# Performance work log

Measured on AMD Instinct MI355X. Metric: run time of the kernel, lower is better.

## Reference

```python
import jax, jax.numpy as jnp
import numpy as np

D = 2048
N_HEAD = 16
D_HEAD = D // N_HEAD
EXP = 4
EPS = 1e-6


def setup_inputs() -> dict:
    key = jax.random.key(0)
    ks = jax.random.split(key, 8)
    b, s = 2, 2048
    scale = 0.02
    return {
        "x": jax.random.normal(ks[0], (b, s, D), dtype=jnp.float32),
        "w_qkv": jax.random.normal(ks[1], (D, 3 * D), dtype=jnp.float32) * scale,
        "w_o": jax.random.normal(ks[2], (D, D), dtype=jnp.float32) * scale,
        "w_up": jax.random.normal(ks[3], (D, EXP * D), dtype=jnp.float32) * scale,
        "w_gate": jax.random.normal(ks[4], (D, EXP * D), dtype=jnp.float32) * scale,
        "w_down": jax.random.normal(ks[5], (EXP * D, D), dtype=jnp.float32) * scale,
        "scale1": jnp.ones((D,), dtype=jnp.float32),
        "scale2": jnp.ones((D,), dtype=jnp.float32),
    }


def _rmsnorm(x, scale):
    rms = jnp.sqrt(jnp.mean(x * x, axis=-1, keepdims=True) + EPS)
    return x / rms * scale


def _attention(x, w_qkv, w_o):
    b, s, d = x.shape
    qkv = x @ w_qkv  # [b, s, 3d]
    q, k, v = jnp.split(qkv, 3, axis=-1)
    # [b, h, s, dh]
    q = q.reshape(b, s, N_HEAD, D_HEAD).transpose(0, 2, 1, 3)
    k = k.reshape(b, s, N_HEAD, D_HEAD).transpose(0, 2, 1, 3)
    v = v.reshape(b, s, N_HEAD, D_HEAD).transpose(0, 2, 1, 3)
    scores = jnp.einsum("bhqd,bhkd->bhqk", q, k) / np.sqrt(D_HEAD).astype(np.float32)
    causal = jnp.tril(jnp.ones((s, s), dtype=bool))
    scores = jnp.where(causal, scores, -jnp.inf)
    attn = jax.nn.softmax(scores, axis=-1)
    out = jnp.einsum("bhqk,bhkd->bhqd", attn, v)
    out = out.transpose(0, 2, 1, 3).reshape(b, s, d)
    return out @ w_o


def _mlp(x, w_up, w_gate, w_down):
    return (x @ w_up * jax.nn.silu(x @ w_gate)) @ w_down


def reference(x, w_qkv, w_o, w_up, w_gate, w_down, scale1, scale2):
    x = x + _attention(_rmsnorm(x, scale1), w_qkv, w_o)
    x = x + _mlp(_rmsnorm(x, scale2), w_up, w_gate, w_down)
    return x
```

## Files before the change

kernel.cpp:

```cpp
#include <hip/hip_runtime.h>

typedef unsigned short u16;
typedef __bf16 bfrag8 __attribute__((ext_vector_type(8)));
typedef float f32x4 __attribute__((ext_vector_type(4)));

#define MFMA16(a, b, c) __builtin_amdgcn_mfma_f32_16x16x32_bf16((a), (b), (c), 0, 0, 0)

static __device__ __forceinline__ u16 bf_bits(float f) {
  unsigned int u = __builtin_bit_cast(unsigned int, f);
  unsigned int r = (u + 0x7fffu + ((u >> 16) & 1u)) >> 16;
  return (u16)r;
}
static __device__ __forceinline__ float f_from_bits(u16 u) {
  unsigned int w = ((unsigned int)u) << 16;
  return __builtin_bit_cast(float, w);
}
static __device__ __forceinline__ void gload16(const void* g, void* l) {
  __builtin_amdgcn_global_load_lds(
      (const __attribute__((address_space(1))) void*)g,
      (__attribute__((address_space(3))) void*)l, 16, 0, 0);
}

__global__ __launch_bounds__(256) void k_transpose_bf16(const float* __restrict__ src,
                                                        u16* __restrict__ dst,
                                                        int K, int N) {
  __shared__ float tile[32][33];
  const int n0 = blockIdx.x * 32;
  const int k0 = blockIdx.y * 32;
  const int t = threadIdx.x;
  const int lr = t >> 5;
  const int lc = t & 31;
#pragma unroll
  for (int i = 0; i < 4; ++i)
    tile[lr + i * 8][lc] = src[(size_t)(k0 + lr + i * 8) * N + n0 + lc];
  __syncthreads();
#pragma unroll
  for (int i = 0; i < 4; ++i)
    dst[(size_t)(n0 + lr + i * 8) * K + k0 + lc] = bf_bits(tile[lc][lr + i * 8]);
}

__global__ __launch_bounds__(256) void k_transpose_v(const u16* __restrict__ qkv,
                                                     u16* __restrict__ vtg) {
  __shared__ u16 tile[32][33];
  const int bh = blockIdx.z, b = bh >> 4, hh = bh & 15;
  const int s0 = blockIdx.x * 32, d0 = blockIdx.y * 32;
  const int t = threadIdx.x;
  const int lr = t >> 5, lc = t & 31;
#pragma unroll
  for (int i = 0; i < 4; ++i)
    tile[lr + i * 8][lc] =
        qkv[(size_t)(b * 2048 + s0 + lr + i * 8) * 6144 + 4096 + hh * 128 + d0 + lc];
  __syncthreads();
#pragma unroll
  for (int i = 0; i < 4; ++i)
    vtg[(size_t)bh * 128 * 2048 + (size_t)(d0 + lr + i * 8) * 2048 + s0 + lc] =
        tile[lc][lr + i * 8];
}

__global__ __launch_bounds__(256) void k_rmsnorm(const float* __restrict__ x,
                                                 const float* __restrict__ sc,
                                                 u16* __restrict__ o) {
  const int row = blockIdx.x;
  const int t = threadIdx.x;
  const float4* x4 = (const float4*)(x + (size_t)row * 2048);
  float4 a = x4[t];
  float4 b = x4[t + 256];
  float ss = a.x * a.x + a.y * a.y + a.z * a.z + a.w * a.w +
             b.x * b.x + b.y * b.y + b.z * b.z + b.w * b.w;
#pragma unroll
  for (int off = 32; off > 0; off >>= 1) ss += __shfl_down(ss, off);
  __shared__ float red[4];
  if ((t & 63) == 0) red[t >> 6] = ss;
  __syncthreads();
  const float inv = rsqrtf((red[0] + red[1] + red[2] + red[3]) * (1.0f / 2048.0f) + 1e-6f);
  const float4* s4 = (const float4*)sc;
  float4 sa = s4[t], sb = s4[t + 256];
  ushort4 pa, pb;
  pa.x = bf_bits(a.x * inv * sa.x); pa.y = bf_bits(a.y * inv * sa.y);
  pa.z = bf_bits(a.z * inv * sa.z); pa.w = bf_bits(a.w * inv * sa.w);
  pb.x = bf_bits(b.x * inv * sb.x); pb.y = bf_bits(b.y * inv * sb.y);
  pb.z = bf_bits(b.z * inv * sb.z); pb.w = bf_bits(b.w * inv * sb.w);
  *(ushort4*)(o + (size_t)row * 2048 + t * 4) = pa;
  *(ushort4*)(o + (size_t)row * 2048 + (t + 256) * 4) = pb;
}

template <int EPI, int K>
__global__ __launch_bounds__(256, 4) void k_gemm(const u16* __restrict__ A,
                                                 const u16* __restrict__ Bt,
                                                 int M, int N,
                                                 float* __restrict__ outF,
                                                 u16* __restrict__ outB,
                                                 const float* __restrict__ resid,
                                                 const u16* __restrict__ gate) {
  __shared__ u16 sm[16384];
  char* smC = (char*)sm;
  const int nbx = gridDim.x;
  const int f = blockIdx.x + nbx * blockIdx.y;
  const int nsl = nbx >> 3;
  const int x = f & 7;
  const int j = f >> 3;
  const int n0 = (x * nsl + (j % nsl)) * 128;
  const int m0 = (j / nsl) * 128;

  const int t = threadIdx.x;
  const int wid = t >> 6, lane = t & 63;
  const int wm = wid >> 1, wn = wid & 1;
  const int l15 = lane & 15, lhi = lane >> 4;
  const int lhi16 = lhi * 16;
  const int swz = (l15 & 7) << 4;

  f32x4 acc[4][4];
#pragma unroll
  for (int i = 0; i < 4; ++i)
#pragma unroll
    for (int j2 = 0; j2 < 4; ++j2) acc[i][j2] = (f32x4){0.f, 0.f, 0.f, 0.f};

  const int sr = lane >> 3;
  const int csw = (((lane & 7) * 16) ^ (sr << 4)) >> 1;
  const u16* Asrc = A + (size_t)(m0 + wid * 32 + sr) * K + csw;
  const u16* Bsrc = Bt + (size_t)(n0 + wid * 32 + sr) * K + csw;
  char* adst = smC + wid * 4096 + lane * 16;
  char* bdst = smC + 16384 + wid * 4096 + lane * 16;

  for (int kt = 0; kt < K / 64; ++kt) {
    __syncthreads();
    const u16* as = Asrc + kt * 64;
    const u16* bs = Bsrc + kt * 64;
#pragma unroll
    for (int c = 0; c < 4; ++c) {
      gload16(as + (size_t)c * 8 * K, adst + c * 1024);
      gload16(bs + (size_t)c * 8 * K, bdst + c * 1024);
    }
    asm volatile("s_waitcnt vmcnt(0)" ::: "memory");
    __syncthreads();

#pragma unroll
    for (int kh = 0; kh < 2; ++kh) {
      bfrag8 a0 = *(const bfrag8*)(smC + (wm * 64 + 0 * 16 + l15) * 128 + ((kh * 64 + lhi16) ^ swz));
      bfrag8 a1 = *(const bfrag8*)(smC + (wm * 64 + 1 * 16 + l15) * 128 + ((kh * 64 + lhi16) ^ swz));
      bfrag8 a2 = *(const bfrag8*)(smC + (wm * 64 + 2 * 16 + l15) * 128 + ((kh * 64 + lhi16) ^ swz));
      bfrag8 a3 = *(const bfrag8*)(smC + (wm * 64 + 3 * 16 + l15) * 128 + ((kh * 64 + lhi16) ^ swz));
      bfrag8 b0 = *(const bfrag8*)(smC + 16384 + (wn * 64 + 0 * 16 + l15) * 128 + ((kh * 64 + lhi16) ^ swz));
      bfrag8 b1 = *(const bfrag8*)(smC + 16384 + (wn * 64 + 1 * 16 + l15) * 128 + ((kh * 64 + lhi16) ^ swz));
      bfrag8 b2 = *(const bfrag8*)(smC + 16384 + (wn * 64 + 2 * 16 + l15) * 128 + ((kh * 64 + lhi16) ^ swz));
      bfrag8 b3 = *(const bfrag8*)(smC + 16384 + (wn * 64 + 3 * 16 + l15) * 128 + ((kh * 64 + lhi16) ^ swz));
      acc[0][0] = MFMA16(a0, b0, acc[0][0]); acc[0][1] = MFMA16(a0, b1, acc[0][1]);
      acc[0][2] = MFMA16(a0, b2, acc[0][2]); acc[0][3] = MFMA16(a0, b3, acc[0][3]);
      acc[1][0] = MFMA16(a1, b0, acc[1][0]); acc[1][1] = MFMA16(a1, b1, acc[1][1]);
      acc[1][2] = MFMA16(a1, b2, acc[1][2]); acc[1][3] = MFMA16(a1, b3, acc[1][3]);
      acc[2][0] = MFMA16(a2, b0, acc[2][0]); acc[2][1] = MFMA16(a2, b1, acc[2][1]);
      acc[2][2] = MFMA16(a2, b2, acc[2][2]); acc[2][3] = MFMA16(a2, b3, acc[2][3]);
      acc[3][0] = MFMA16(a3, b0, acc[3][0]); acc[3][1] = MFMA16(a3, b1, acc[3][1]);
      acc[3][2] = MFMA16(a3, b2, acc[3][2]); acc[3][3] = MFMA16(a3, b3, acc[3][3]);
    }
  }

#pragma unroll
  for (int i = 0; i < 4; ++i) {
#pragma unroll
    for (int j2 = 0; j2 < 4; ++j2) {
      const int mr = m0 + wm * 64 + i * 16 + lhi * 4;
      const int nc = n0 + wn * 64 + j2 * 16 + l15;
#pragma unroll
      for (int r = 0; r < 4; ++r) {
        const size_t idx = (size_t)(mr + r) * N + nc;
        const float v = acc[i][j2][r];
        if (EPI == 0) {
          outB[idx] = bf_bits(v);
        } else if (EPI == 1) {
          outF[idx] = resid[idx] + v;
        } else {
          float g = f_from_bits(gate[idx]);
          float s = g / (1.f + __expf(-g));
          outB[idx] = bf_bits(v * s);
        }
      }
    }
  }
}

__global__ __launch_bounds__(512) void k_attn(const u16* __restrict__ qkv,
                                              const u16* __restrict__ vtg,
                                              u16* __restrict__ out) {
  const int S = 2048, LD = 6144;
  const float scale = 0.0883883476483184405f;
  const int bh = blockIdx.y;
  const int b = bh >> 4, hh = bh & 15;
  const int qt = (b == 0) ? (15 - (int)blockIdx.x) : (int)blockIdx.x;
  const int t = threadIdx.x;
  const int wave = t >> 6, lane = t & 63;
  const int l15 = lane & 15, lhi = lane >> 4;
  const int lhi16 = lhi * 16;
  const int swz = (l15 & 7) << 4;

  __shared__ u16 Kt[64 * 128];
  __shared__ u16 Vt[128 * 64];
  __shared__ u16 Pl[8][16][72];
  char* KtC = (char*)Kt;
  char* VtC = (char*)Vt;

  const int qrow = qt * 128 + wave * 16 + l15;
  const size_t qoff = (size_t)(b * S + qrow) * LD + hh * 128 + lhi * 8;
  bfrag8 qf[4];
#pragma unroll
  for (int ks = 0; ks < 4; ++ks) qf[ks] = *(const bfrag8*)(qkv + qoff + ks * 32);

  f32x4 oacc[8];
#pragma unroll
  for (int j = 0; j < 8; ++j) oacc[j] = (f32x4){0.f, 0.f, 0.f, 0.f};
  float m_i[4], l_i[4];
#pragma unroll
  for (int r = 0; r < 4; ++r) { m_i[r] = -INFINITY; l_i[r] = 0.f; }

  const int q_my = qt * 128 + wave * 16 + lhi * 4;
  const int q_wave_last = qt * 128 + wave * 16 + 15;

  const int keyA = t >> 4, keyB = 32 + (t >> 4);
  const int oK = (t & 15) * 16;
  const int dA = t >> 3, dB = 64 + (t >> 3);
  const int oV = (t & 7) * 16;
  const u16* kbase = qkv + (size_t)(b * S) * LD + 2048 + hh * 128;
  const u16* vbase = vtg + (size_t)bh * 128 * S;
  const u16* ksrcA = kbase + (size_t)keyA * LD + ((oK ^ ((keyA & 7) << 4)) >> 1);
  const u16* ksrcB = kbase + (size_t)keyB * LD + ((oK ^ ((keyB & 7) << 4)) >> 1);
  const u16* vsrcA = vbase + (size_t)dA * S + ((oV ^ ((dA & 7) << 4)) >> 1);
  const u16* vsrcB = vbase + (size_t)dB * S + ((oV ^ ((dB & 7) << 4)) >> 1);
  const unsigned int ldso0 = wave * 1024 + lane * 16;
  const unsigned int ldso1 = 8192 + wave * 1024 + lane * 16;
  const size_t kstep = (size_t)64 * LD;

  const int kt_max = 2 * qt + 1;
  for (int kt = 0; kt <= kt_max; ++kt) {
    __syncthreads();
    gload16(ksrcA + (size_t)kt * kstep, KtC + ldso0);
    gload16(ksrcB + (size_t)kt * kstep, KtC + ldso1);
    gload16(vsrcA + kt * 64, VtC + ldso0);
    gload16(vsrcB + kt * 64, VtC + ldso1);
    __syncthreads();

    if (kt * 64 <= q_wave_last) {
      f32x4 sfr[4];
#pragma unroll
      for (int j = 0; j < 4; ++j) {
        sfr[j] = (f32x4){0.f, 0.f, 0.f, 0.f};
        const int krow = j * 16 + l15;
#pragma unroll
        for (int ks = 0; ks < 4; ++ks) {
          bfrag8 kf = *(const bfrag8*)(KtC + krow * 256 + ((ks * 64 + lhi16) ^ swz));
          sfr[j] = MFMA16(qf[ks], kf, sfr[j]);
        }
      }
      float sv[4][4], rmax[4];
#pragma unroll
      for (int r = 0; r < 4; ++r) rmax[r] = -INFINITY;
#pragma unroll
      for (int j = 0; j < 4; ++j) {
        const int key = kt * 64 + j * 16 + l15;
#pragma unroll
        for (int r = 0; r < 4; ++r) {
          float v = sfr[j][r] * scale;
          v = (key <= q_my + r) ? v : -INFINITY;
          sv[j][r] = v;
          rmax[r] = fmaxf(rmax[r], v);
        }
      }
#pragma unroll
      for (int r = 0; r < 4; ++r) {
        float v = rmax[r];
        v = fmaxf(v, __shfl_xor(v, 1));
        v = fmaxf(v, __shfl_xor(v, 2));
        v = fmaxf(v, __shfl_xor(v, 4));
        v = fmaxf(v, __shfl_xor(v, 8));
        rmax[r] = v;
      }
      float alpha[4], rsum[4];
#pragma unroll
      for (int r = 0; r < 4; ++r) {
        float mn = fmaxf(m_i[r], rmax[r]);
        alpha[r] = __expf(m_i[r] - mn);
        m_i[r] = mn;
        rsum[r] = 0.f;
      }
#pragma unroll
      for (int j = 0; j < 4; ++j) {
#pragma unroll
        for (int r = 0; r < 4; ++r) {
          float p = __expf(sv[j][r] - m_i[r]);
          rsum[r] += p;
          Pl[wave][lhi * 4 + r][j * 16 + l15] = bf_bits(p);
        }
      }
#pragma unroll
      for (int r = 0; r < 4; ++r) {
        float v = rsum[r];
        v += __shfl_xor(v, 1); v += __shfl_xor(v, 2);
        v += __shfl_xor(v, 4); v += __shfl_xor(v, 8);
        l_i[r] = l_i[r] * alpha[r] + v;
      }
#pragma unroll
      for (int j = 0; j < 8; ++j)
#pragma unroll
        for (int r = 0; r < 4; ++r) oacc[j][r] *= alpha[r];

#pragma unroll
      for (int ks2 = 0; ks2 < 2; ++ks2) {
        bfrag8 pf = *(const bfrag8*)&Pl[wave][l15][ks2 * 32 + lhi * 8];
#pragma unroll
        for (int j = 0; j < 8; ++j) {
          const int d = j * 16 + l15;
          bfrag8 vf = *(const bfrag8*)(VtC + d * 128 + ((ks2 * 64 + lhi16) ^ swz));
          oacc[j] = MFMA16(pf, vf, oacc[j]);
        }
      }
    }
  }

#pragma unroll
  for (int r = 0; r < 4; ++r) {
    const float inv = 1.f / l_i[r];
    const size_t tok = (size_t)b * S + qt * 128 + wave * 16 + lhi * 4 + r;
#pragma unroll
    for (int j = 0; j < 8; ++j)
      out[tok * 2048 + hh * 128 + j * 16 + l15] = bf_bits(oacc[j][r] * inv);
  }
}

extern "C" void kernel_launch(void* const* d_in, const int* in_sizes, int n_in,
                              void* d_out, int out_size, void* d_ws, size_t ws_size,
                              hipStream_t stream) {
  (void)in_sizes; (void)n_in; (void)out_size; (void)ws_size;
  const float* x      = (const float*)d_in[0];
  const float* w_qkv  = (const float*)d_in[1];
  const float* w_o    = (const float*)d_in[2];
  const float* w_up   = (const float*)d_in[3];
  const float* w_gate = (const float*)d_in[4];
  const float* w_down = (const float*)d_in[5];
  const float* scale1 = (const float*)d_in[6];
  const float* scale2 = (const float*)d_in[7];
  float* out = (float*)d_out;

  u16* B       = (u16*)d_ws;
  u16* wqkvT   = B;
  u16* woT     = wqkvT  + (size_t)6144 * 2048;
  u16* wgateT  = woT    + (size_t)2048 * 2048;
  u16* wupT    = wgateT + (size_t)8192 * 2048;
  u16* wdownT  = wupT   + (size_t)8192 * 2048;
  u16* xn      = wdownT + (size_t)2048 * 8192;
  u16* qkvb    = xn     + (size_t)4096 * 2048;
  u16* attnb   = qkvb   + (size_t)4096 * 6144;
  float* y1    = (float*)(attnb + (size_t)4096 * 2048);
  u16* vtg     = (u16*)y1;
  u16* gbuf    = qkvb;
  u16* hbuf    = wqkvT;

  dim3 blk(256);
  k_transpose_bf16<<<dim3(192, 64), blk, 0, stream>>>(w_qkv,  wqkvT,  2048, 6144);
  k_transpose_bf16<<<dim3(64, 64),  blk, 0, stream>>>(w_o,    woT,    2048, 2048);
  k_transpose_bf16<<<dim3(256, 64), blk, 0, stream>>>(w_gate, wgateT, 2048, 8192);
  k_transpose_bf16<<<dim3(256, 64), blk, 0, stream>>>(w_up,   wupT,   2048, 8192);
  k_transpose_bf16<<<dim3(64, 256), blk, 0, stream>>>(w_down, wdownT, 8192, 2048);

  k_rmsnorm<<<4096, blk, 0, stream>>>(x, scale1, xn);
  k_gemm<0, 2048><<<dim3(48, 32), blk, 0, stream>>>(xn, wqkvT, 4096, 6144, nullptr, qkvb, nullptr, nullptr);
  k_transpose_v<<<dim3(64, 4, 32), blk, 0, stream>>>(qkvb, vtg);
  k_attn<<<dim3(16, 32), dim3(512), 0, stream>>>(qkvb, vtg, attnb);
  k_gemm<1, 2048><<<dim3(16, 32), blk, 0, stream>>>(attnb, woT, 4096, 2048, y1, nullptr, x, nullptr);
  k_rmsnorm<<<4096, blk, 0, stream>>>(y1, scale2, xn);
  k_gemm<0, 2048><<<dim3(64, 32), blk, 0, stream>>>(xn, wgateT, 4096, 8192, nullptr, gbuf, nullptr, nullptr);
  k_gemm<2, 2048><<<dim3(64, 32), blk, 0, stream>>>(xn, wupT, 4096, 8192, nullptr, hbuf, nullptr, gbuf);
  k_gemm<1, 8192><<<dim3(16, 32), blk, 0, stream>>>(hbuf, wdownT, 4096, 2048, out, nullptr, y1, nullptr);
}
```

Before: 886.0 us.

## Fuse gate and up projections into one dual-accumulator GEMM with SiLU epilogue

Replaces the separate gate GEMM and up GEMM with a single kernel. It streams each A tile once alongside matching tiles of both weight matrices and keeps two accumulator sets per wave. The SiLU gating is applied in registers before writing the bf16 hidden buffer, so the intermediate gate tensor is no longer written to and read back from global memory, and one kernel launch is dropped. In exchange, the doubled accumulator state raises register pressure and the LDS tile grows to 48KB, which may limit occupancy.

```diff
diff --git a/kernel.cpp b/kernel.cpp
--- a/kernel.cpp
+++ b/kernel.cpp
@@ -179,6 +179,112 @@
   }
 }
 
+template <int K>
+__global__ __launch_bounds__(256, 2) void k_gemm_mlp(const u16* __restrict__ A,
+                                                     const u16* __restrict__ Bg,
+                                                     const u16* __restrict__ Bu,
+                                                     int N,
+                                                     u16* __restrict__ outB) {
+  __shared__ u16 sm[24576];
+  char* smC = (char*)sm;
+  const int nbx = gridDim.x;
+  const int f = blockIdx.x + nbx * blockIdx.y;
+  const int nsl = nbx >> 3;
+  const int x = f & 7;
+  const int j = f >> 3;
+  const int n0 = (x * nsl + (j % nsl)) * 128;
+  const int m0 = (j / nsl) * 128;
+
+  const int t = threadIdx.x;
+  const int wid = t >> 6, lane = t & 63;
+  const int wm = wid >> 1, wn = wid & 1;
+  const int l15 = lane & 15, lhi = lane >> 4;
+  const int lhi16 = lhi * 16;
+  const int swz = (l15 & 7) << 4;
+
+  f32x4 accg[4][4], accu[4][4];
+#pragma unroll
+  for (int i = 0; i < 4; ++i)
+#pragma unroll
+    for (int j2 = 0; j2 < 4; ++j2) {
+      accg[i][j2] = (f32x4){0.f, 0.f, 0.f, 0.f};
+      accu[i][j2] = (f32x4){0.f, 0.f, 0.f, 0.f};
+    }
+
+  const int sr = lane >> 3;
+  const int csw = (((lane & 7) * 16) ^ (sr << 4)) >> 1;
+  const u16* Asrc = A + (size_t)(m0 + wid * 32 + sr) * K + csw;
+  const u16* Bgsrc = Bg + (size_t)(n0 + wid * 32 + sr) * K + csw;
+  const u16* Busrc = Bu + (size_t)(n0 + wid * 32 + sr) * K + csw;
+  char* adst = smC + wid * 4096 + lane * 16;
+  char* bgdst = smC + 16384 + wid * 4096 + lane * 16;
+  char* budst = smC + 32768 + wid * 4096 + lane * 16;
+
+  for (int kt = 0; kt < K / 64; ++kt) {
+    __syncthreads();
+    const u16* as = Asrc + kt * 64;
+    const u16* gs = Bgsrc + kt * 64;
+    const u16* us = Busrc + kt * 64;
+#pragma unroll
+    for (int c = 0; c < 4; ++c) {
+      gload16(as + (size_t)c * 8 * K, adst + c * 1024);
+      gload16(gs + (size_t)c * 8 * K, bgdst + c * 1024);
+      gload16(us + (size_t)c * 8 * K, budst + c * 1024);
+    }
+    asm volatile("s_waitcnt vmcnt(0)" ::: "memory");
+    __syncthreads();
+
+#pragma unroll
+    for (int kh = 0; kh < 2; ++kh) {
+      const int ko = (kh * 64 + lhi16);
+      bfrag8 a0 = *(const bfrag8*)(smC + (wm * 64 + 0 * 16 + l15) * 128 + (ko ^ swz));
+      bfrag8 a1 = *(const bfrag8*)(smC + (wm * 64 + 1 * 16 + l15) * 128 + (ko ^ swz));
+      bfrag8 a2 = *(const bfrag8*)(smC + (wm * 64 + 2 * 16 + l15) * 128 + (ko ^ swz));
+      bfrag8 a3 = *(const bfrag8*)(smC + (wm * 64 + 3 * 16 + l15) * 128 + (ko ^ swz));
+      bfrag8 g0 = *(const bfrag8*)(smC + 16384 + (wn * 64 + 0 * 16 + l15) * 128 + (ko ^ swz));
+      bfrag8 g1 = *(const bfrag8*)(smC + 16384 + (wn * 64 + 1 * 16 + l15) * 128 + (ko ^ swz));
+      bfrag8 g2 = *(const bfrag8*)(smC + 16384 + (wn * 64 + 2 * 16 + l15) * 128 + (ko ^ swz));
+      bfrag8 g3 = *(const bfrag8*)(smC + 16384 + (wn * 64 + 3 * 16 + l15) * 128 + (ko ^ swz));
+      accg[0][0] = MFMA16(a0, g0, accg[0][0]); accg[0][1] = MFMA16(a0, g1, accg[0][1]);
+      accg[0][2] = MFMA16(a0, g2, accg[0][2]); accg[0][3] = MFMA16(a0, g3, accg[0][3]);
+      accg[1][0] = MFMA16(a1, g0, accg[1][0]); accg[1][1] = MFMA16(a1, g1, accg[1][1]);
+      accg[1][2] = MFMA16(a1, g2, accg[1][2]); accg[1][3] = MFMA16(a1, g3, accg[1][3]);
+      accg[2][0] = MFMA16(a2, g0, accg[2][0]); accg[2][1] = MFMA16(a2, g1, accg[2][1]);
+      accg[2][2] = MFMA16(a2, g2, accg[2][2]); accg[2][3] = MFMA16(a2, g3, accg[2][3]);
+      accg[3][0] = MFMA16(a3, g0, accg[3][0]); accg[3][1] = MFMA16(a3, g1, accg[3][1]);
+      accg[3][2] = MFMA16(a3, g2, accg[3][2]); accg[3][3] = MFMA16(a3, g3, accg[3][3]);
+      bfrag8 u0 = *(const bfrag8*)(smC + 32768 + (wn * 64 + 0 * 16 + l15) * 128 + (ko ^ swz));
+      bfrag8 u1 = *(const bfrag8*)(smC + 32768 + (wn * 64 + 1 * 16 + l15) * 128 + (ko ^ swz));
+      bfrag8 u2 = *(const bfrag8*)(smC + 32768 + (wn * 64 + 2 * 16 + l15) * 128 + (ko ^ swz));
+      bfrag8 u3 = *(const bfrag8*)(smC + 32768 + (wn * 64 + 3 * 16 + l15) * 128 + (ko ^ swz));
+      accu[0][0] = MFMA16(a0, u0, accu[0][0]); accu[0][1] = MFMA16(a0, u1, accu[0][1]);
+      accu[0][2] = MFMA16(a0, u2, accu[0][2]); accu[0][3] = MFMA16(a0, u3, accu[0][3]);
+      accu[1][0] = MFMA16(a1, u0, accu[1][0]); accu[1][1] = MFMA16(a1, u1, accu[1][1]);
+      accu[1][2] = MFMA16(a1, u2, accu[1][2]); accu[1][3] = MFMA16(a1, u3, accu[1][3]);
+      accu[2][0] = MFMA16(a2, u0, accu[2][0]); accu[2][1] = MFMA16(a2, u1, accu[2][1]);
+      accu[2][2] = MFMA16(a2, u2, accu[2][2]); accu[2][3] = MFMA16(a2, u3, accu[2][3]);
+      accu[3][0] = MFMA16(a3, u0, accu[3][0]); accu[3][1] = MFMA16(a3, u1, accu[3][1]);
+      accu[3][2] = MFMA16(a3, u2, accu[3][2]); accu[3][3] = MFMA16(a3, u3, accu[3][3]);
+    }
+  }
+
+#pragma unroll
+  for (int i = 0; i < 4; ++i) {
+#pragma unroll
+    for (int j2 = 0; j2 < 4; ++j2) {
+      const int mr = m0 + wm * 64 + i * 16 + lhi * 4;
+      const int nc = n0 + wn * 64 + j2 * 16 + l15;
+#pragma unroll
+      for (int r = 0; r < 4; ++r) {
+        const float g = accg[i][j2][r];
+        const float u = accu[i][j2][r];
+        const float s = g / (1.f + __expf(-g));
+        outB[(size_t)(mr + r) * N + nc] = bf_bits(u * s);
+      }
+    }
+  }
+}
+
 __global__ __launch_bounds__(512) void k_attn(const u16* __restrict__ qkv,
                                               const u16* __restrict__ vtg,
                                               u16* __restrict__ out) {
@@ -350,8 +456,7 @@
   u16* attnb   = qkvb   + (size_t)4096 * 6144;
   float* y1    = (float*)(attnb + (size_t)4096 * 2048);
   u16* vtg     = (u16*)y1;
-  u16* gbuf    = qkvb;
-  u16* hbuf    = wqkvT;
+  u16* hbuf    = qkvb;
 
   dim3 blk(256);
   k_transpose_bf16<<<dim3(192, 64), blk, 0, stream>>>(w_qkv,  wqkvT,  2048, 6144);
@@ -366,7 +471,6 @@
   k_attn<<<dim3(16, 32), dim3(512), 0, stream>>>(qkvb, vtg, attnb);
   k_gemm<1, 2048><<<dim3(16, 32), blk, 0, stream>>>(attnb, woT, 4096, 2048, y1, nullptr, x, nullptr);
   k_rmsnorm<<<4096, blk, 0, stream>>>(y1, scale2, xn);
-  k_gemm<0, 2048><<<dim3(64, 32), blk, 0, stream>>>(xn, wgateT, 4096, 8192, nullptr, gbuf, nullptr, nullptr);
-  k_gemm<2, 2048><<<dim3(64, 32), blk, 0, stream>>>(xn, wupT, 4096, 8192, nullptr, hbuf, nullptr, gbuf);
+  k_gemm_mlp<2048><<<dim3(64, 32), blk, 0, stream>>>(xn, wgateT, wupT, 8192, hbuf);
   k_gemm<1, 8192><<<dim3(16, 32), blk, 0, stream>>>(hbuf, wdownT, 4096, 2048, out, nullptr, y1, nullptr);
 }
```

After: 865.4 us. 2.3% less time.
